# Kernel optimization log

Measured on AMD Instinct MI355X. Metric: run time of the kernel, lower is better.

Reference implementation:

```python
import jax, jax.numpy as jnp
import numpy as np

VOCAB, E, H = 32000, 256, 256
B, T = 64, 2048


def setup_inputs() -> dict:
    key = jax.random.key(0)
    ks = jax.random.split(key, 6)
    X = jax.random.randint(ks[0], (B, T), 0, VOCAB)
    emb = jax.random.normal(ks[1], (VOCAB, E), dtype=jnp.float32)
    W_qrnn = jax.random.normal(ks[2], (E, 3 * H), dtype=jnp.float32) / np.sqrt(E)
    b_qrnn = jnp.zeros((3 * H,), dtype=jnp.float32)
    c0 = jax.random.normal(ks[3], (B, H), dtype=jnp.float32)
    W_out = jax.random.normal(ks[4], (H, 1), dtype=jnp.float32) / np.sqrt(H)
    b_out = jnp.zeros((1,), dtype=jnp.float32)
    return {"X": X, "emb": emb, "W_qrnn": W_qrnn, "b_qrnn": b_qrnn,
            "c0": c0, "W_out": W_out, "b_out": b_out}


def reference(X, emb, W_qrnn, b_qrnn, c0, W_out, b_out):
    # Embedding lookup: [B,T] -> [B,T,E]; permute to seq-major [T,B,E]
    x = jnp.transpose(emb[X], (1, 0, 2))
    # QRNN window=1 gate projection: all timesteps in one GEMM, [T,B,3H]
    g = jnp.einsum('tbe,ef->tbf', x, W_qrnn) + b_qrnn
    z, f, o = jnp.split(g, 3, axis=-1)
    z = jnp.tanh(z)
    f = jax.nn.sigmoid(f)
    o = jax.nn.sigmoid(o)

    # fo-pooling recurrence: c_t = f_t * c_{t-1} + (1 - f_t) * z_t
    def step(c, zf):
        z_t, f_t = zf
        c = f_t * c + (1.0 - f_t) * z_t
        return c, c

    _, cs = jax.lax.scan(step, c0, (z, f))  # cs: [T,B,H]
    h = o * cs                              # h_t = o_t * c_t
    hn = h[-1]                              # last timestep, [B,H]
    return hn @ W_out + b_out               # [B,1]
```

## Files before the change

### kernel.cpp

```cpp
#include <hip/hip_runtime.h>
#include <hip/hip_bf16.h>
#include <math.h>

#define EDIM 256
#define HDIM 256
#define BDIM 64
#define TDIM 2048
#define NC   64
#define TC   32
#define CPB  4

typedef __attribute__((ext_vector_type(8)))  short  short8;
typedef __attribute__((ext_vector_type(4)))  float  floatx4;
typedef __attribute__((ext_vector_type(4)))  unsigned int uintx4;

__device__ __forceinline__ unsigned short f2bf(float f) {
    unsigned int u = __float_as_uint(f);
    u += 0x7FFFu + ((u >> 16) & 1u);
    return (unsigned short)(u >> 16);
}
__device__ __forceinline__ unsigned int pk2(float a, float b) {
    return (unsigned int)f2bf(a) | ((unsigned int)f2bf(b) << 16);
}
__device__ __forceinline__ float sigm(float x) {
    return __builtin_amdgcn_rcpf(1.f + __expf(-x));
}
__device__ __forceinline__ float tanh_fast(float x) {
    return fmaf(-2.f, __builtin_amdgcn_rcpf(1.f + __expf(2.f * x)), 1.f);
}

__global__ __launch_bounds__(256) void qrnn_pack(
    const float* __restrict__ Wq, const float* __restrict__ emb,
    unsigned short* __restrict__ Wp, unsigned short* __restrict__ ebf,
    int mode)
{
    const int bx = blockIdx.x;
    if (bx < 256) {
        const int nt = (bx >> 3) & 7;
        const int hg = bx >> 6;
        const int ks = bx & 7;
        const int t = threadIdx.x;
        const int lane = t >> 2, pj = t & 3;
        const int col = lane & 15, q = lane >> 4;
        const int h = hg * 64 + (nt & 3) * 16 + col;
        const int c = (nt < 4) ? h : (HDIM + h);
        const int k = ks * 32 + q * 8 + pj * 2;
        unsigned int v = pk2(Wq[k * (3 * HDIM) + c], Wq[(k + 1) * (3 * HDIM) + c]);
        *(unsigned int*)(Wp + (size_t)bx * 512 + lane * 8 + pj * 2) = v;
    } else if (mode == 1) {
        size_t i = ((size_t)(bx - 256) * 256 + threadIdx.x) * 8;
        floatx4 a = *(const floatx4*)(emb + i);
        floatx4 b = *(const floatx4*)(emb + i + 4);
        uintx4 o = {pk2(a.x, a.y), pk2(a.z, a.w), pk2(b.x, b.y), pk2(b.z, b.w)};
        *(uintx4*)(ebf + i) = o;
    }
}

template<int MODE>
__global__ __launch_bounds__(512, 2) void qrnn_mfma(
    const int* __restrict__ X, const float* __restrict__ emb,
    const unsigned short* __restrict__ ebf, const unsigned short* __restrict__ Wp,
    const float* __restrict__ bq, float* __restrict__ wsA, float* __restrict__ wsB)
{
    __shared__ __align__(16) short Bsh[32768];

    const int tid = threadIdx.x;
    const int cg = blockIdx.x, bg = blockIdx.y, hg = blockIdx.z;
    const int lane = tid & 63, w = tid >> 6;
    const int col = lane & 15, q = lane >> 4;

    const unsigned short* wpb = Wp + (size_t)hg * 32768;
#pragma unroll
    for (int i = 0; i < 8; ++i) {
        const int ch = w * 8 + i;
        __builtin_amdgcn_global_load_lds(
            (const __attribute__((address_space(1))) unsigned int*)(wpb + ch * 512 + lane * 8),
            (__attribute__((address_space(3))) unsigned int*)(Bsh + ch * 512),
            16, 0, 0);
    }

    const int b0 = bg * 8 + w;
    int xid[CPB][2];
#pragma unroll
    for (int c = 0; c < CPB; ++c)
#pragma unroll
        for (int mt = 0; mt < 2; ++mt)
            xid[c][mt] = X[b0 * TDIM + (cg * CPB + c) * TC + mt * 16 + col];

    const int hbase = hg * 64;
    float bz[4], bff[4];
#pragma unroll
    for (int nt = 0; nt < 4; ++nt) {
        bz[nt]  = bq[hbase + nt * 16 + col];
        bff[nt] = bq[HDIM + hbase + nt * 16 + col];
    }

    short8 abuf[3][2];
    auto fetchA = [&](int c, int ks, int slot) {
#pragma unroll
        for (int mt = 0; mt < 2; ++mt) {
            if constexpr (MODE == 1) {
                abuf[slot][mt] = *(const short8*)(ebf + (size_t)xid[c][mt] * EDIM + q * 8 + ks * 32);
            } else {
                const float* ap = emb + (size_t)xid[c][mt] * EDIM + q * 8 + ks * 32;
                floatx4 f0 = *(const floatx4*)ap;
                floatx4 f1 = *(const floatx4*)(ap + 4);
                uintx4 p = {pk2(f0.x, f0.y), pk2(f0.z, f0.w),
                            pk2(f1.x, f1.y), pk2(f1.z, f1.w)};
                abuf[slot][mt] = *(short8*)&p;
            }
        }
    };

    floatx4 acc[2][8];
#pragma unroll
    for (int mt = 0; mt < 2; ++mt)
#pragma unroll
        for (int nt = 0; nt < 8; ++nt) acc[mt][nt] = (floatx4){0.f, 0.f, 0.f, 0.f};

    fetchA(0, 0, 0);
    fetchA(0, 1, 1);
    __syncthreads();

#pragma unroll
    for (int c = 0; c < CPB; ++c) {
#pragma unroll
        for (int ks = 0; ks < 8; ++ks) {
            const int s = c * 8 + ks;
            if (s + 2 < CPB * 8)
                fetchA((s + 2) >> 3, (s + 2) & 7, (s + 2) % 3);
            short8 bf[8];
#pragma unroll
            for (int nt = 0; nt < 8; ++nt)
                bf[nt] = *(const short8*)(Bsh + (nt * 8 + ks) * 512 + lane * 8);
            const int sl = s % 3;
#pragma unroll
            for (int nt = 0; nt < 8; ++nt)
#pragma unroll
                for (int mt = 0; mt < 2; ++mt)
                    acc[mt][nt] = __builtin_amdgcn_mfma_f32_16x16x32_bf16(abuf[sl][mt], bf[nt], acc[mt][nt], 0, 0, 0);
        }

        const int cc = cg * CPB + c;
        float Af[4], Bf[4];
#pragma unroll
        for (int nt = 0; nt < 4; ++nt) {
            float Aseg[2], Bseg[2];
#pragma unroll
            for (int mt = 0; mt < 2; ++mt) {
                float Ac = 1.f, Bc = 0.f;
#pragma unroll
                for (int j = 0; j < 4; ++j) {
                    float z = tanh_fast(acc[mt][nt][j] + bz[nt]);
                    float f = sigm(acc[mt][nt + 4][j] + bff[nt]);
                    Ac = f * Ac;
                    Bc = fmaf(f, Bc, (1.f - f) * z);
                }
                Aseg[mt] = Ac; Bseg[mt] = Bc;
            }
#pragma unroll
            for (int st = 0; st < 2; ++st) {
                const int msk = 16 << st;
                const bool self_earlier = ((q >> st) & 1) == 0;
#pragma unroll
                for (int mt = 0; mt < 2; ++mt) {
                    float Ap = __shfl_xor(Aseg[mt], msk, 64);
                    float Bp = __shfl_xor(Bseg[mt], msk, 64);
                    Bseg[mt] = self_earlier ? fmaf(Ap, Bseg[mt], Bp)
                                            : fmaf(Aseg[mt], Bp, Bseg[mt]);
                    Aseg[mt] = Aseg[mt] * Ap;
                }
            }
            Af[nt] = Aseg[0] * Aseg[1];
            Bf[nt] = fmaf(Aseg[1], Bseg[0], Bseg[1]);
        }

        float As = (q == 0) ? Af[0] : (q == 1) ? Af[1] : (q == 2) ? Af[2] : Af[3];
        float Bs = (q == 0) ? Bf[0] : (q == 1) ? Bf[1] : (q == 2) ? Bf[2] : Bf[3];

        const size_t r0 = ((size_t)cc * BDIM + b0) * HDIM + hbase + lane;
        wsA[r0] = As;
        wsB[r0] = Bs;

#pragma unroll
        for (int mt = 0; mt < 2; ++mt)
#pragma unroll
            for (int nt = 0; nt < 8; ++nt) acc[mt][nt] = (floatx4){0.f, 0.f, 0.f, 0.f};
    }
}

__global__ __launch_bounds__(256) void qrnn_combine(
    const float* __restrict__ wsA, const float* __restrict__ wsB,
    const float* __restrict__ c0, const int* __restrict__ X,
    const float* __restrict__ emb, const float* __restrict__ Wq,
    const float* __restrict__ bq, const float* __restrict__ Wout,
    const float* __restrict__ bout, float* __restrict__ out)
{
    const int b = blockIdx.x;
    const int h = threadIdx.x;

    float c = c0[b * HDIM + h];
    for (int c8 = 0; c8 < NC; c8 += 8) {
        float a[8], bb[8];
#pragma unroll
        for (int i = 0; i < 8; ++i) {
            size_t base = ((size_t)(c8 + i) * BDIM + b) * HDIM + h;
            a[i]  = wsA[base];
            bb[i] = wsB[base];
        }
#pragma unroll
        for (int i = 0; i < 8; ++i) c = fmaf(a[i], c, bb[i]);
    }

    __shared__ float xs[EDIM];
    int idx = X[b * TDIM + (TDIM - 1)];
    xs[h] = emb[(size_t)idx * EDIM + h];
    __syncthreads();

    float acc = 0.f;
#pragma unroll 16
    for (int e = 0; e < EDIM; ++e)
        acc = fmaf(xs[e], Wq[e * (3 * HDIM) + 2 * HDIM + h], acc);

    float o  = 1.f / (1.f + expf(-(acc + bq[2 * HDIM + h])));
    float hn = o * c;

    __shared__ float red[HDIM];
    red[h] = hn * Wout[h];
    __syncthreads();
    for (int s = HDIM / 2; s > 0; s >>= 1) {
        if (h < s) red[h] += red[h + s];
        __syncthreads();
    }
    if (h == 0) out[b] = red[0] + bout[0];
}

extern "C" void kernel_launch(void* const* d_in, const int* in_sizes, int n_in,
                              void* d_out, int out_size, void* d_ws, size_t ws_size,
                              hipStream_t stream) {
    const int*   X    = (const int*)d_in[0];
    const float* emb  = (const float*)d_in[1];
    const float* Wq   = (const float*)d_in[2];
    const float* bq   = (const float*)d_in[3];
    const float* c0   = (const float*)d_in[4];
    const float* Wout = (const float*)d_in[5];
    const float* bout = (const float*)d_in[6];
    float* out = (float*)d_out;

    float* wsA = (float*)d_ws;
    float* wsB = wsA + (size_t)NC * BDIM * HDIM;
    unsigned short* Wp  = (unsigned short*)(wsB + (size_t)NC * BDIM * HDIM);
    unsigned short* ebf = Wp + (size_t)256 * 512;

    const size_t wsAB = (size_t)2 * NC * BDIM * HDIM * 4;
    const size_t wpsz = (size_t)256 * 512 * 2;
    const size_t need1 = wsAB + wpsz + (size_t)32000 * EDIM * 2;
    const int mode = (ws_size >= need1) ? 1 : 0;

    const int gather_blocks = (mode == 1) ? (32000 * EDIM / 8) / 256 : 0;
    qrnn_pack<<<256 + gather_blocks, 256, 0, stream>>>(Wq, emb, Wp, ebf, mode);

    dim3 g(NC / CPB, BDIM / 8, HDIM / 64);
    if (mode == 1) qrnn_mfma<1><<<g, 512, 0, stream>>>(X, emb, ebf, Wp, bq, wsA, wsB);
    else           qrnn_mfma<0><<<g, 512, 0, stream>>>(X, emb, ebf, Wp, bq, wsA, wsB);

    qrnn_combine<<<BDIM, 256, 0, stream>>>(wsA, wsB, c0, X, emb, Wq, bq, Wout, bout, out);
}
```

Baseline: 150.3 us.

## Fuse combine into MFMA kernel via last-block atomic counter and deepen A prefetch

Removes the separate combine kernel launch. Each batch group keeps an atomic counter, and the last of its 64 blocks runs the sequential chunk scan, the output-gate dot product and the final reduction for its 8 batch rows. The A-operand prefetch ring also grows from 3 to 5 slots, so gathers are issued 4 steps ahead instead of 2. This adds a memset, release/acquire fences, and a serial tail done by only 8 blocks, which could become the critical path. The deeper prefetch also raises register pressure under launch_bounds(512,2).

```diff
diff --git a/kernel.cpp b/kernel.cpp
--- a/kernel.cpp
+++ b/kernel.cpp
@@ -60,7 +60,11 @@
 __global__ __launch_bounds__(512, 2) void qrnn_mfma(
     const int* __restrict__ X, const float* __restrict__ emb,
     const unsigned short* __restrict__ ebf, const unsigned short* __restrict__ Wp,
-    const float* __restrict__ bq, float* __restrict__ wsA, float* __restrict__ wsB)
+    const float* __restrict__ bq, float* __restrict__ wsA, float* __restrict__ wsB,
+    unsigned int* __restrict__ cnt,
+    const float* __restrict__ c0, const float* __restrict__ Wq,
+    const float* __restrict__ Wout, const float* __restrict__ bout,
+    float* __restrict__ out)
 {
     __shared__ __align__(16) short Bsh[32768];
 
@@ -95,7 +99,7 @@
         bff[nt] = bq[HDIM + hbase + nt * 16 + col];
     }
 
-    short8 abuf[3][2];
+    short8 abuf[5][2];
     auto fetchA = [&](int c, int ks, int slot) {
 #pragma unroll
         for (int mt = 0; mt < 2; ++mt) {
@@ -120,6 +124,8 @@
 
     fetchA(0, 0, 0);
     fetchA(0, 1, 1);
+    fetchA(0, 2, 2);
+    fetchA(0, 3, 3);
     __syncthreads();
 
 #pragma unroll
@@ -127,13 +133,13 @@
 #pragma unroll
         for (int ks = 0; ks < 8; ++ks) {
             const int s = c * 8 + ks;
-            if (s + 2 < CPB * 8)
-                fetchA((s + 2) >> 3, (s + 2) & 7, (s + 2) % 3);
+            if (s + 4 < CPB * 8)
+                fetchA((s + 4) >> 3, (s + 4) & 7, (s + 4) % 5);
             short8 bf[8];
 #pragma unroll
             for (int nt = 0; nt < 8; ++nt)
                 bf[nt] = *(const short8*)(Bsh + (nt * 8 + ks) * 512 + lane * 8);
-            const int sl = s % 3;
+            const int sl = s % 5;
 #pragma unroll
             for (int nt = 0; nt < 8; ++nt)
 #pragma unroll
@@ -187,52 +193,60 @@
 #pragma unroll
             for (int nt = 0; nt < 8; ++nt) acc[mt][nt] = (floatx4){0.f, 0.f, 0.f, 0.f};
     }
-}
-
-__global__ __launch_bounds__(256) void qrnn_combine(
-    const float* __restrict__ wsA, const float* __restrict__ wsB,
-    const float* __restrict__ c0, const int* __restrict__ X,
-    const float* __restrict__ emb, const float* __restrict__ Wq,
-    const float* __restrict__ bq, const float* __restrict__ Wout,
-    const float* __restrict__ bout, float* __restrict__ out)
-{
-    const int b = blockIdx.x;
-    const int h = threadIdx.x;
-
-    float c = c0[b * HDIM + h];
-    for (int c8 = 0; c8 < NC; c8 += 8) {
-        float a[8], bb[8];
-#pragma unroll
-        for (int i = 0; i < 8; ++i) {
-            size_t base = ((size_t)(c8 + i) * BDIM + b) * HDIM + h;
-            a[i]  = wsA[base];
-            bb[i] = wsB[base];
-        }
-#pragma unroll
-        for (int i = 0; i < 8; ++i) c = fmaf(a[i], c, bb[i]);
-    }
-
-    __shared__ float xs[EDIM];
-    int idx = X[b * TDIM + (TDIM - 1)];
-    xs[h] = emb[(size_t)idx * EDIM + h];
+
     __syncthreads();
-
-    float acc = 0.f;
+    volatile int* flag = (volatile int*)Bsh;
+    if (tid == 0) {
+        __builtin_amdgcn_fence(__ATOMIC_RELEASE, "agent");
+        unsigned int old = __hip_atomic_fetch_add(&cnt[bg], 1u,
+                               __ATOMIC_ACQ_REL, __HIP_MEMORY_SCOPE_AGENT);
+        *flag = (old == 63u) ? 1 : 0;
+    }
+    __syncthreads();
+    if (*flag == 0) return;
+    __builtin_amdgcn_fence(__ATOMIC_ACQUIRE, "agent");
+
+    float* shf = (float*)Bsh;
+    const int bi = tid >> 8;
+    const int h  = tid & 255;
+#pragma unroll 1
+    for (int rep = 0; rep < 4; ++rep) {
+        const int b = bg * 8 + rep * 2 + bi;
+
+        float cacc = c0[b * HDIM + h];
+        for (int c8 = 0; c8 < NC; c8 += 8) {
+            float a[8], bb[8];
+#pragma unroll
+            for (int i = 0; i < 8; ++i) {
+                size_t base = ((size_t)(c8 + i) * BDIM + b) * HDIM + h;
+                a[i]  = wsA[base];
+                bb[i] = wsB[base];
+            }
+#pragma unroll
+            for (int i = 0; i < 8; ++i) cacc = fmaf(a[i], cacc, bb[i]);
+        }
+
+        int idx = X[b * TDIM + (TDIM - 1)];
+        shf[bi * 256 + h] = emb[(size_t)idx * EDIM + h];
+        __syncthreads();
+
+        float dacc = 0.f;
 #pragma unroll 16
-    for (int e = 0; e < EDIM; ++e)
-        acc = fmaf(xs[e], Wq[e * (3 * HDIM) + 2 * HDIM + h], acc);
-
-    float o  = 1.f / (1.f + expf(-(acc + bq[2 * HDIM + h])));
-    float hn = o * c;
-
-    __shared__ float red[HDIM];
-    red[h] = hn * Wout[h];
-    __syncthreads();
-    for (int s = HDIM / 2; s > 0; s >>= 1) {
-        if (h < s) red[h] += red[h + s];
+        for (int e = 0; e < EDIM; ++e)
+            dacc = fmaf(shf[bi * 256 + e], Wq[e * (3 * HDIM) + 2 * HDIM + h], dacc);
+
+        float o  = 1.f / (1.f + expf(-(dacc + bq[2 * HDIM + h])));
+        float hn = o * cacc;
+
+        shf[512 + tid] = hn * Wout[h];
         __syncthreads();
-    }
-    if (h == 0) out[b] = red[0] + bout[0];
+        for (int s = HDIM / 2; s > 0; s >>= 1) {
+            if (h < s) shf[512 + tid] += shf[512 + tid + s];
+            __syncthreads();
+        }
+        if (h == 0) out[b] = shf[512 + bi * 256] + bout[0];
+        __syncthreads();
+    }
 }
 
 extern "C" void kernel_launch(void* const* d_in, const int* in_sizes, int n_in,
@@ -247,22 +261,27 @@
     const float* bout = (const float*)d_in[6];
     float* out = (float*)d_out;
 
-    float* wsA = (float*)d_ws;
+    unsigned int* cnt = (unsigned int*)d_ws;
+    float* wsA = (float*)((char*)d_ws + 256);
     float* wsB = wsA + (size_t)NC * BDIM * HDIM;
     unsigned short* Wp  = (unsigned short*)(wsB + (size_t)NC * BDIM * HDIM);
     unsigned short* ebf = Wp + (size_t)256 * 512;
 
     const size_t wsAB = (size_t)2 * NC * BDIM * HDIM * 4;
     const size_t wpsz = (size_t)256 * 512 * 2;
-    const size_t need1 = wsAB + wpsz + (size_t)32000 * EDIM * 2;
+    const size_t need1 = 256 + wsAB + wpsz + (size_t)32000 * EDIM * 2;
     const int mode = (ws_size >= need1) ? 1 : 0;
+
+    (void)hipMemsetAsync(cnt, 0, 32, stream);
 
     const int gather_blocks = (mode == 1) ? (32000 * EDIM / 8) / 256 : 0;
     qrnn_pack<<<256 + gather_blocks, 256, 0, stream>>>(Wq, emb, Wp, ebf, mode);
 
     dim3 g(NC / CPB, BDIM / 8, HDIM / 64);
-    if (mode == 1) qrnn_mfma<1><<<g, 512, 0, stream>>>(X, emb, ebf, Wp, bq, wsA, wsB);
-    else           qrnn_mfma<0><<<g, 512, 0, stream>>>(X, emb, ebf, Wp, bq, wsA, wsB);
-
-    qrnn_combine<<<BDIM, 256, 0, stream>>>(wsA, wsB, c0, X, emb, Wq, bq, Wout, bout, out);
-}
+    if (mode == 1)
+        qrnn_mfma<1><<<g, 512, 0, stream>>>(X, emb, ebf, Wp, bq, wsA, wsB,
+                                            cnt, c0, Wq, Wout, bout, out);
+    else
+        qrnn_mfma<0><<<g, 512, 0, stream>>>(X, emb, ebf, Wp, bq, wsA, wsB,
+                                            cnt, c0, Wq, Wout, bout, out);
+}
```

Result: slower. 194.9 us (+29.7%).
